# Optimization experiments

Hardware: AMD Instinct MI355X
Metric: run time of the kernel (lower is better)

Reference implementation:

```python
import jax, jax.numpy as jnp
import numpy as np

N = 50000          # nodes
E = 400000         # edges (before self-loops)
F_IN = 64          # node features
H = 256            # hidden_dim
HEADS = 8
HD = 32            # head dim (hidden_dim // 8)
L = 4              # num_layers
G = 64             # num graphs
NGF = 32           # graph features per graph
NC = 2             # classes
EPS = 1e-5


def _bn(x, g, b):
    # BatchNorm1d with batch statistics (training-mode math, no dropout)
    mu = jnp.mean(x, axis=0)
    var = jnp.var(x, axis=0)
    return (x - mu) * jax.lax.rsqrt(var + EPS) * g + b


def _gat(x, src, dst, W, a_src, a_dst, bias):
    # PyG GATConv math (self-loops already included in src/dst)
    h = (x @ W).reshape(N, HEADS, HD)                      # [N,8,32]
    as_n = jnp.sum(h * a_src, axis=-1)                     # [N,8]
    ad_n = jnp.sum(h * a_dst, axis=-1)                     # [N,8]
    e = jax.nn.leaky_relu(as_n[src] + ad_n[dst], 0.2)      # [E',8]
    m = jax.ops.segment_max(e, dst, num_segments=N)        # per-dest softmax
    ex = jnp.exp(e - m[dst])
    den = jax.ops.segment_sum(ex, dst, num_segments=N)
    alpha = ex / den[dst]                                  # [E',8]
    out = jax.ops.segment_sum(alpha[:, :, None] * h[src], dst, num_segments=N)
    return out.reshape(N, HEADS * HD) + bias


def setup_inputs() -> dict:
    key = jax.random.key(0)
    ks = jax.random.split(key, 20)
    s = 0.05
    inp = {
        "x": jax.random.normal(ks[0], (N, F_IN), jnp.float32),
        "edge_index": jax.random.randint(ks[1], (2, E), 0, N, jnp.int32),
        "batch": jnp.sort(jax.random.randint(ks[2], (N,), 0, G, jnp.int32)),
        "graph_features": jax.random.normal(ks[3], (G * NGF,), jnp.float32),
        # node encoder
        "W_enc": jax.random.normal(ks[4], (F_IN, H), jnp.float32) * s,
        "b_enc": jnp.zeros((H,), jnp.float32),
        "g_enc": jnp.ones((H,), jnp.float32),
        "be_enc": jnp.zeros((H,), jnp.float32),
        # GAT layers (stacked over L layers)
        "Wg": jax.random.normal(ks[5], (L, H, H), jnp.float32) * s,
        "att_src": jax.random.normal(ks[6], (L, HEADS, HD), jnp.float32) * s,
        "att_dst": jax.random.normal(ks[7], (L, HEADS, HD), jnp.float32) * s,
        "bg": jnp.zeros((L, H), jnp.float32),
        "bn_g": jnp.ones((L, H), jnp.float32),
        "bn_b": jnp.zeros((L, H), jnp.float32),
        # classifier: (3H + NGF) -> 2H -> H -> NC
        "W1": jax.random.normal(ks[8], (3 * H + NGF, 2 * H), jnp.float32) * s,
        "b1": jnp.zeros((2 * H,), jnp.float32),
        "g1": jnp.ones((2 * H,), jnp.float32),
        "be1": jnp.zeros((2 * H,), jnp.float32),
        "W2": jax.random.normal(ks[9], (2 * H, H), jnp.float32) * s,
        "b2": jnp.zeros((H,), jnp.float32),
        "g2": jnp.ones((H,), jnp.float32),
        "be2": jnp.zeros((H,), jnp.float32),
        "W3": jax.random.normal(ks[10], (H, NC), jnp.float32) * s,
        "b3": jnp.zeros((NC,), jnp.float32),
    }
    return inp


def reference(x, edge_index, batch, graph_features, W_enc, b_enc, g_enc, be_enc,
              Wg, att_src, att_dst, bg, bn_g, bn_b,
              W1, b1, g1, be1, W2, b2, g2, be2, W3, b3):
    gf = graph_features.reshape(G, NGF)
    # add self loops (PyG GATConv default)
    loop = jnp.arange(N, dtype=edge_index.dtype)
    src = jnp.concatenate([edge_index[0], loop])
    dst = jnp.concatenate([edge_index[1], loop])

    h = jax.nn.relu(_bn(x @ W_enc + b_enc, g_enc, be_enc))  # node encoder
    for i in range(L):
        h_in = h
        h = _gat(h, src, dst, Wg[i], att_src[i], att_dst[i], bg[i])
        h = jax.nn.relu(_bn(h, bn_g[i], bn_b[i]))
        if i > 0 and i % 2 == 0:
            h = h + h_in

    # concat pooling: mean / max / sum over graphs
    cnt = jax.ops.segment_sum(jnp.ones((N,), h.dtype), batch, num_segments=G)
    s = jax.ops.segment_sum(h, batch, num_segments=G)
    mean = s / cnt[:, None]
    mx = jax.ops.segment_max(h, batch, num_segments=G)
    pooled = jnp.concatenate([mean, mx, s], axis=1)         # [G, 3H]

    z = jnp.concatenate([pooled, gf], axis=1)               # [G, 3H+NGF]
    z = jax.nn.relu(_bn(z @ W1 + b1, g1, be1))
    z = jax.nn.relu(_bn(z @ W2 + b2, g2, be2))
    return z @ W3 + b3                                      # [G, NC]
```

## Files before the change

kernel.cpp:

```cpp
#include <hip/hip_runtime.h>

#define NN 50000
#define MPAD 50048
#define EE 400000
#define EP 450000
#define FIN 64
#define HH 256
#define GG 64
#define NGFD 32
#define SB 782
#define RB 64

typedef __attribute__((ext_vector_type(8))) _Float16 f16x8;
typedef __attribute__((ext_vector_type(8))) unsigned short u16x8;
typedef __attribute__((ext_vector_type(4))) float f32x4;

__device__ __forceinline__ unsigned short f2h(float f) {
  _Float16 h = (_Float16)f;
  return __builtin_bit_cast(unsigned short, h);
}
__device__ __forceinline__ float h2f(unsigned short s) {
  _Float16 h = __builtin_bit_cast(_Float16, s);
  return (float)h;
}

__global__ void k_init_deg(int* deg) {
  int i = blockIdx.x * 256 + threadIdx.x;
  if (i < NN) deg[i] = 1;
}
__global__ void k_hist(const int* __restrict__ dst, int* __restrict__ deg) {
  int e = blockIdx.x * 256 + threadIdx.x;
  if (e < EE) atomicAdd(&deg[dst[e]], 1);
}
__global__ void k_scan1(const int* __restrict__ deg, int* __restrict__ offs, int* __restrict__ aux) {
  __shared__ int sd[256];
  int b = blockIdx.x, t = threadIdx.x;
  int base = b * 1024 + t * 4;
  int v0 = 0, v1 = 0, v2 = 0, v3 = 0;
  if (base + 0 < NN) v0 = deg[base + 0];
  if (base + 1 < NN) v1 = deg[base + 1];
  if (base + 2 < NN) v2 = deg[base + 2];
  if (base + 3 < NN) v3 = deg[base + 3];
  sd[t] = v0 + v1 + v2 + v3;
  __syncthreads();
  for (int off = 1; off < 256; off <<= 1) {
    int x = (t >= off) ? sd[t - off] : 0;
    __syncthreads();
    sd[t] += x;
    __syncthreads();
  }
  if (t == 255) aux[b] = sd[255];
  int run = (t == 0) ? 0 : sd[t - 1];
  if (base + 0 < NN) offs[base + 0] = run; run += v0;
  if (base + 1 < NN) offs[base + 1] = run; run += v1;
  if (base + 2 < NN) offs[base + 2] = run; run += v2;
  if (base + 3 < NN) offs[base + 3] = run;
}
__global__ void k_scan2(int* aux, int nb) {
  if (threadIdx.x == 0 && blockIdx.x == 0) {
    int s = 0;
    for (int i = 0; i < nb; ++i) { int t = aux[i]; aux[i] = s; s += t; }
    aux[nb] = s;
  }
}
__global__ void k_scan3(int* __restrict__ offs, const int* __restrict__ aux) {
  int b = blockIdx.x, t = threadIdx.x;
  int base = b * 1024 + t * 4;
  int add = aux[b];
  #pragma unroll
  for (int i = 0; i < 4; ++i)
    if (base + i < NN) offs[base + i] += add;
  if (b == 0 && t == 0) offs[NN] = aux[gridDim.x];
}
__global__ void k_scatter(const int* __restrict__ srcA, const int* __restrict__ dstA,
                          int* __restrict__ cur, int* __restrict__ ssrc) {
  int e = blockIdx.x * 256 + threadIdx.x;
  if (e < EE) { int p = atomicAdd(&cur[dstA[e]], 1); ssrc[p] = srcA[e]; }
}
__global__ void k_scatter_self(int* __restrict__ cur, int* __restrict__ ssrc) {
  int i = blockIdx.x * 256 + threadIdx.x;
  if (i < NN) { int p = atomicAdd(&cur[i], 1); ssrc[p] = i; }
}

__global__ void k_bounds(const int* __restrict__ batch, int* __restrict__ start) {
  int g = threadIdx.x;
  if (g > GG) return;
  int lo = 0, hi = NN;
  while (lo < hi) { int mid = (lo + hi) >> 1; if (batch[mid] < g) lo = mid + 1; else hi = mid; }
  start[g] = lo;
}

__global__ void k_prepW(const float* __restrict__ W, unsigned short* __restrict__ WT, int K, int N) {
  __shared__ float tile[32][33];
  int l = blockIdx.z;
  const float* Wp = W + (size_t)l * K * N;
  unsigned short* Tp = WT + (size_t)l * K * N;
  int n0 = blockIdx.x * 32, k0 = blockIdx.y * 32;
  int tx = threadIdx.x & 31, ty = threadIdx.x >> 5;
  #pragma unroll
  for (int rr = 0; rr < 32; rr += 8) {
    int k = k0 + ty + rr, n = n0 + tx;
    if (k < K && n < N) tile[ty + rr][tx] = Wp[(size_t)k * N + n];
  }
  __syncthreads();
  #pragma unroll
  for (int rr = 0; rr < 32; rr += 8) {
    int n = n0 + ty + rr, k = k0 + tx;
    if (n < N && k < K) Tp[(size_t)n * K + k] = f2h(tile[tx][ty + rr]);
  }
}

__global__ void k_cvt_x(const float* __restrict__ x, unsigned short* __restrict__ xb) {
  size_t i = ((size_t)blockIdx.x * 256 + threadIdx.x) * 4;
  if (i >= (size_t)NN * FIN) return;
  float4 v = *reinterpret_cast<const float4*>(x + i);
  ushort4 o;
  o.x = f2h(v.x); o.y = f2h(v.y); o.z = f2h(v.z); o.w = f2h(v.w);
  *reinterpret_cast<ushort4*>(xb + i) = o;
}

__global__ __launch_bounds__(256) void k_mfma(const unsigned short* __restrict__ A,
                                              const unsigned short* __restrict__ BT,
                                              unsigned short* __restrict__ Cb, int K) {
  __shared__ unsigned short Tile[128 * 132];
  unsigned short* As = Tile;
  unsigned short* Bs = Tile + 8192;
  const int t = threadIdx.x;
  const int w = t >> 6, l = t & 63;
  const int row0 = blockIdx.x * 128;
  const int col0 = blockIdx.y * 128;
  const int wm = w & 1, wn = w >> 1;

  f32x4 acc[4][4];
  #pragma unroll
  for (int i = 0; i < 4; ++i)
    #pragma unroll
    for (int j = 0; j < 4; ++j) acc[i][j] = (f32x4){0.f, 0.f, 0.f, 0.f};

  const int lrow = w * 8 + (l >> 3);
  const int ksrc_sh = ((l & 7) ^ (lrow & 7)) << 3;

  for (int k0 = 0; k0 < K; k0 += 64) {
    #pragma unroll
    for (int rd = 0; rd < 4; ++rd) {
      int r = rd * 32 + lrow;
      const unsigned short* ga = A + (size_t)(row0 + r) * K + k0 + ksrc_sh;
      __builtin_amdgcn_global_load_lds(
          (const __attribute__((address_space(1))) void*)ga,
          (__attribute__((address_space(3))) void*)(As + (size_t)(rd * 32 + w * 8) * 64),
          16, 0, 0);
    }
    #pragma unroll
    for (int rd = 0; rd < 4; ++rd) {
      int r = rd * 32 + lrow;
      const unsigned short* gb = BT + (size_t)(col0 + r) * K + k0 + ksrc_sh;
      __builtin_amdgcn_global_load_lds(
          (const __attribute__((address_space(1))) void*)gb,
          (__attribute__((address_space(3))) void*)(Bs + (size_t)(rd * 32 + w * 8) * 64),
          16, 0, 0);
    }
    __syncthreads();

    const char* AsB = (const char*)As;
    const char* BsB = (const char*)Bs;
    #pragma unroll
    for (int ks = 0; ks < 2; ++ks) {
      f16x8 af[4], bfr[4];
      #pragma unroll
      for (int i = 0; i < 4; ++i) {
        int ar = wm * 64 + i * 16 + (l & 15);
        int ab = ar * 128 + ((ks * 64 + (l >> 4) * 16) ^ ((ar & 7) << 4));
        af[i] = *(const f16x8*)(AsB + ab);
        int br = wn * 64 + i * 16 + (l & 15);
        int bb = br * 128 + ((ks * 64 + (l >> 4) * 16) ^ ((br & 7) << 4));
        bfr[i] = *(const f16x8*)(BsB + bb);
      }
      #pragma unroll
      for (int i = 0; i < 4; ++i)
        #pragma unroll
        for (int j = 0; j < 4; ++j)
          acc[i][j] = __builtin_amdgcn_mfma_f32_16x16x32_f16(af[i], bfr[j], acc[i][j], 0, 0, 0);
    }
    __syncthreads();
  }

  #pragma unroll
  for (int i = 0; i < 4; ++i) {
    int lrow2 = wm * 64 + i * 16 + ((l >> 4) * 4);
    #pragma unroll
    for (int j = 0; j < 4; ++j) {
      int lcol = wn * 64 + j * 16 + (l & 15);
      #pragma unroll
      for (int r = 0; r < 4; ++r)
        Tile[(lrow2 + r) * 132 + lcol] = f2h(acc[i][j][r]);
    }
  }
  __syncthreads();
  #pragma unroll
  for (int u = 0; u < 8; ++u) {
    int idx = u * 256 + t;
    int row = idx >> 4;
    int cc  = (idx & 15) * 8;
    int gr = row0 + row;
    if (gr < NN) {
      u16x8 v = *reinterpret_cast<const u16x8*>(&Tile[row * 132 + cc]);
      *reinterpret_cast<u16x8*>(Cb + (size_t)gr * HH + col0 + cc) = v;
    }
  }
}

__global__ void k_attdot(const unsigned short* __restrict__ hp, const float* __restrict__ a_s,
                         const float* __restrict__ a_d, float* __restrict__ asn,
                         float* __restrict__ adn) {
  int lane = threadIdx.x & 63;
  int n = blockIdx.x * 4 + (threadIdx.x >> 6);
  if (n >= NN) return;
  ushort4 v = *reinterpret_cast<const ushort4*>(hp + (size_t)n * HH + lane * 4);
  float4 s4 = *reinterpret_cast<const float4*>(a_s + lane * 4);
  float4 d4 = *reinterpret_cast<const float4*>(a_d + lane * 4);
  float x0 = h2f(v.x), x1 = h2f(v.y), x2 = h2f(v.z), x3 = h2f(v.w);
  float ps = x0 * s4.x + x1 * s4.y + x2 * s4.z + x3 * s4.w;
  float pd = x0 * d4.x + x1 * d4.y + x2 * d4.z + x3 * d4.w;
  ps += __shfl_xor(ps, 1); ps += __shfl_xor(ps, 2); ps += __shfl_xor(ps, 4);
  pd += __shfl_xor(pd, 1); pd += __shfl_xor(pd, 2); pd += __shfl_xor(pd, 4);
  if ((lane & 7) == 0) {
    asn[n * 8 + (lane >> 3)] = ps;
    adn[n * 8 + (lane >> 3)] = pd;
  }
}

__global__ __launch_bounds__(256) void k_gat_agg(const int* __restrict__ offs, const int* __restrict__ ssrc,
                                                 const float* __restrict__ asn, const float* __restrict__ adn,
                                                 const unsigned short* __restrict__ hp,
                                                 unsigned short* __restrict__ outp) {
  int lane = threadIdx.x & 63;
  int n = blockIdx.x * 4 + (threadIdx.x >> 6);
  if (n >= NN) return;
  int hd = lane >> 3;
  float adh = adn[n * 8 + hd];
  int e0 = offs[n], e1 = offs[n + 1];
  float den = 0.f;
  float4 acc = make_float4(0.f, 0.f, 0.f, 0.f);

  auto step = [&](float av, ushort4 hv) {
    float e = fmaxf(av, 0.2f * av);
    float p = __expf(fminf(e, 40.f));
    den += p;
    acc.x += p * h2f(hv.x);
    acc.y += p * h2f(hv.y);
    acc.z += p * h2f(hv.z);
    acc.w += p * h2f(hv.w);
  };

  int k = e0;
  for (; k + 8 <= e1; k += 8) {
    int s[8];
    ushort4 hv[8];
    float a[8];
    #pragma unroll
    for (int u = 0; u < 8; ++u) s[u] = ssrc[k + u];
    #pragma unroll
    for (int u = 0; u < 8; ++u)
      hv[u] = *reinterpret_cast<const ushort4*>(hp + (size_t)s[u] * HH + lane * 4);
    #pragma unroll
    for (int u = 0; u < 8; ++u) a[u] = asn[s[u] * 8 + hd] + adh;
    #pragma unroll
    for (int u = 0; u < 8; ++u) step(a[u], hv[u]);
  }
  for (; k + 4 <= e1; k += 4) {
    int s0 = ssrc[k], s1 = ssrc[k + 1], s2 = ssrc[k + 2], s3 = ssrc[k + 3];
    ushort4 h0 = *reinterpret_cast<const ushort4*>(hp + (size_t)s0 * HH + lane * 4);
    ushort4 h1 = *reinterpret_cast<const ushort4*>(hp + (size_t)s1 * HH + lane * 4);
    ushort4 h2 = *reinterpret_cast<const ushort4*>(hp + (size_t)s2 * HH + lane * 4);
    ushort4 h3 = *reinterpret_cast<const ushort4*>(hp + (size_t)s3 * HH + lane * 4);
    float a0 = asn[s0 * 8 + hd] + adh;
    float a1 = asn[s1 * 8 + hd] + adh;
    float a2 = asn[s2 * 8 + hd] + adh;
    float a3 = asn[s3 * 8 + hd] + adh;
    step(a0, h0); step(a1, h1); step(a2, h2); step(a3, h3);
  }
  for (; k < e1; ++k) {
    int s = ssrc[k];
    ushort4 hv = *reinterpret_cast<const ushort4*>(hp + (size_t)s * HH + lane * 4);
    float av = asn[s * 8 + hd] + adh;
    step(av, hv);
  }
  float rden = 1.f / den;
  ushort4 o;
  o.x = f2h(acc.x * rden); o.y = f2h(acc.y * rden);
  o.z = f2h(acc.z * rden); o.w = f2h(acc.w * rden);
  *reinterpret_cast<ushort4*>(outp + (size_t)n * HH + lane * 4) = o;
}

__global__ void k_cstat_h(const unsigned short* __restrict__ x, float* __restrict__ pst) {
  int c = threadIdx.x, b = blockIdx.x;
  int r0 = b * 64, r1 = min(r0 + 64, NN);
  float s = 0.f, q = 0.f;
  for (int r = r0; r < r1; ++r) {
    float v = h2f(x[(size_t)r * HH + c]);
    s += v; q += v * v;
  }
  pst[b * 512 + c] = s;
  pst[b * 512 + 256 + c] = q;
}
__global__ void k_redstat1(const float* __restrict__ pst, float* __restrict__ pst2) {
  int t = threadIdx.x, p = blockIdx.x;
  int b0 = p * 13, b1 = min(b0 + 13, SB);
  float s0 = 0.f, s1 = 0.f;
  for (int b = b0; b < b1; ++b) {
    s0 += pst[b * 512 + t];
    s1 += pst[b * 512 + 256 + t];
  }
  pst2[p * 512 + t] = s0;
  pst2[p * 512 + 256 + t] = s1;
}
__global__ void k_redstat2(const float* __restrict__ pst2, float* __restrict__ stats) {
  int c = blockIdx.x * 256 + threadIdx.x;
  float s = 0.f;
  #pragma unroll
  for (int b = 0; b < RB; ++b) s += pst2[b * 512 + c];
  stats[c] = s;
}

__global__ void k_bnap_h(const unsigned short* __restrict__ x, const float* __restrict__ stats,
                         const float* __restrict__ g, const float* __restrict__ b,
                         const unsigned short* res, unsigned short* __restrict__ ybf) {
  size_t i = ((size_t)blockIdx.x * 256 + threadIdx.x) * 4;
  if (i >= (size_t)NN * HH) return;
  ushort4 v = *reinterpret_cast<const ushort4*>(x + i);
  int c = (int)(i & 255);
  const float invN = 1.f / (float)NN;
  float vv[4] = {h2f(v.x), h2f(v.y), h2f(v.z), h2f(v.w)};
  float rv[4] = {0.f, 0.f, 0.f, 0.f};
  if (res) {
    ushort4 r4 = *reinterpret_cast<const ushort4*>(res + i);
    rv[0] = h2f(r4.x); rv[1] = h2f(r4.y); rv[2] = h2f(r4.z); rv[3] = h2f(r4.w);
  }
  float o[4];
  #pragma unroll
  for (int j = 0; j < 4; ++j) {
    int cc = c + j;
    float mean = stats[cc] * invN;
    float var = stats[HH + cc] * invN - mean * mean;
    float rs = rsqrtf(var + 1e-5f);
    float val = (vv[j] - mean) * rs * g[cc] + b[cc];
    val = fmaxf(val, 0.f) + rv[j];
    o[j] = val;
  }
  ushort4 bo;
  bo.x = f2h(o[0]); bo.y = f2h(o[1]); bo.z = f2h(o[2]); bo.w = f2h(o[3]);
  *reinterpret_cast<ushort4*>(ybf + i) = bo;
}

__global__ void k_pool(const unsigned short* __restrict__ h, const int* __restrict__ batch,
                       float* __restrict__ gsum, float* __restrict__ gmax) {
  int c = threadIdx.x;
  int r0 = blockIdx.x * 64, r1 = min(r0 + 64, NN);
  if (r0 >= r1) return;
  int curg = batch[r0];
  float s = 0.f, mx = 0.f;
  for (int r = r0; r < r1; ++r) {
    int g = batch[r];
    if (g != curg) {
      atomicAdd(&gsum[curg * HH + c], s);
      atomicMax((int*)&gmax[curg * HH + c], __float_as_int(mx));
      s = 0.f; mx = 0.f; curg = g;
    }
    float v = h2f(h[(size_t)r * HH + c]);
    s += v; mx = fmaxf(mx, v);
  }
  atomicAdd(&gsum[curg * HH + c], s);
  atomicMax((int*)&gmax[curg * HH + c], __float_as_int(mx));
}
__global__ void k_buildz(const float* __restrict__ gsum, const float* __restrict__ gmax,
                         const int* __restrict__ start, const float* __restrict__ gf,
                         float* __restrict__ z) {
  int g = blockIdx.x;
  float invc = 1.f / (float)(start[g + 1] - start[g]);
  for (int c = threadIdx.x; c < 800; c += 256) {
    float v;
    if (c < 256)      v = gsum[g * HH + c] * invc;
    else if (c < 512) v = gmax[g * HH + (c - 256)];
    else if (c < 768) v = gsum[g * HH + (c - 512)];
    else              v = gf[g * NGFD + (c - 768)];
    z[g * 800 + c] = v;
  }
}

__global__ __launch_bounds__(256) void k_linsplit(const float* __restrict__ zin,
                                                  const float* __restrict__ W,
                                                  float* __restrict__ pacc, int K, int OC) {
  __shared__ float zs[64][65];
  int t = threadIdx.x;
  int kc = blockIdx.y, k0 = kc * 64;
  int kmax = min(64, K - k0);
  for (int idx = t; idx < 64 * 64; idx += 256) {
    int r = idx >> 6, k = idx & 63;
    zs[r][k] = (k < kmax) ? zin[(size_t)r * K + k0 + k] : 0.f;
  }
  __syncthreads();
  int jl = t & 15, rq = t >> 4;
  int j = blockIdx.x * 16 + jl;
  float acc[4] = {0.f, 0.f, 0.f, 0.f};
  int k = 0;
  for (; k + 8 <= kmax; k += 8) {
    float wv[8];
    #pragma unroll
    for (int u = 0; u < 8; ++u) wv[u] = W[(size_t)(k0 + k + u) * OC + j];
    #pragma unroll
    for (int u = 0; u < 8; ++u)
      #pragma unroll
      for (int rr = 0; rr < 4; ++rr) acc[rr] += zs[rq * 4 + rr][k + u] * wv[u];
  }
  for (; k < kmax; ++k) {
    float wv = W[(size_t)(k0 + k) * OC + j];
    #pragma unroll
    for (int rr = 0; rr < 4; ++rr) acc[rr] += zs[rq * 4 + rr][k] * wv;
  }
  float* pp = pacc + ((size_t)kc * OC + j) * 64 + rq * 4;
  #pragma unroll
  for (int rr = 0; rr < 4; ++rr) pp[rr] = acc[rr];
}

__global__ __launch_bounds__(64) void k_linred(const float* __restrict__ pacc,
                                               const float* __restrict__ g,
                                               const float* __restrict__ be,
                                               float* __restrict__ zout, int OC, int KC) {
  int j = blockIdx.x, r = threadIdx.x;
  float s = 0.f;
  for (int kc = 0; kc < KC; ++kc) s += pacc[((size_t)kc * OC + j) * 64 + r];
  float S = s, Q = s * s;
  #pragma unroll
  for (int off = 32; off >= 1; off >>= 1) {
    S += __shfl_xor(S, off);
    Q += __shfl_xor(Q, off);
  }
  float mu = S * (1.f / 64.f);
  float var = Q * (1.f / 64.f) - mu * mu;
  float scv = rsqrtf(var + 1e-5f) * g[j];
  float sh = be[j] - mu * scv;
  zout[(size_t)r * OC + j] = fmaxf(s * scv + sh, 0.f);
}

__global__ void k_final(const float* __restrict__ z2, const float* __restrict__ W3,
                        const float* __restrict__ b3, float* __restrict__ out) {
  int t = threadIdx.x;
  if (t >= 128) return;
  int i = t >> 1, j = t & 1;
  float acc = b3[j];
  for (int k = 0; k < 256; ++k) acc += z2[i * 256 + k] * W3[k * 2 + j];
  out[i * 2 + j] = acc;
}

extern "C" void kernel_launch(void* const* d_in, const int* in_sizes, int n_in,
                              void* d_out, int out_size, void* d_ws, size_t ws_size,
                              hipStream_t stream) {
  const float* x      = (const float*)d_in[0];
  const int*   ei     = (const int*)d_in[1];
  const int*   batch  = (const int*)d_in[2];
  const float* gf     = (const float*)d_in[3];
  const float* W_enc  = (const float*)d_in[4];
  const float* g_enc  = (const float*)d_in[6];
  const float* be_enc = (const float*)d_in[7];
  const float* Wg     = (const float*)d_in[8];
  const float* att_s  = (const float*)d_in[9];
  const float* att_d  = (const float*)d_in[10];
  const float* bn_g   = (const float*)d_in[12];
  const float* bn_b   = (const float*)d_in[13];
  const float* W1     = (const float*)d_in[14];
  const float* g1     = (const float*)d_in[16];
  const float* be1    = (const float*)d_in[17];
  const float* W2     = (const float*)d_in[18];
  const float* g2     = (const float*)d_in[20];
  const float* be2    = (const float*)d_in[21];
  const float* W3     = (const float*)d_in[22];
  const float* b3     = (const float*)d_in[23];
  float* out = (float*)d_out;

  char* w = (char*)d_ws;
  auto alloc = [&](size_t bytes) { char* p = w; w += (bytes + 255) & ~(size_t)255; return p; };
  unsigned short* Cc_h = (unsigned short*)alloc((size_t)MPAD * HH * 2);
  unsigned short* A_bf = (unsigned short*)alloc((size_t)MPAD * HH * 2);
  unsigned short* hp   = (unsigned short*)alloc((size_t)MPAD * HH * 2);
  unsigned short* x_bf = (unsigned short*)alloc((size_t)MPAD * FIN * 2);
  float* asn  = (float*)alloc((size_t)NN * 8 * 4);
  float* adn  = (float*)alloc((size_t)NN * 8 * 4);
  int*   deg  = (int*)alloc((size_t)NN * 4);
  int*   offs = (int*)alloc((size_t)(NN + 1) * 4);
  int*   cur  = (int*)alloc((size_t)NN * 4);
  int*   ssrc = (int*)alloc((size_t)EP * 4);
  float* pst  = (float*)alloc((size_t)SB * 512 * 4);
  float* pst2 = (float*)alloc((size_t)RB * 512 * 4);
  float* stats= (float*)alloc(512 * 4);
  int*   aux  = (int*)alloc(64 * 4);
  int*   start= (int*)alloc(65 * 4);
  unsigned short* WencT = (unsigned short*)alloc((size_t)HH * FIN * 2);
  unsigned short* WgT   = (unsigned short*)alloc((size_t)4 * HH * HH * 2);
  float* gsum = (float*)alloc((size_t)GG * HH * 4);
  float* gmax = (float*)alloc((size_t)GG * HH * 4);
  float* zb   = (float*)alloc((size_t)GG * 800 * 4);
  float* z1   = (float*)alloc((size_t)GG * 512 * 4);
  float* z2   = (float*)alloc((size_t)GG * 256 * 4);
  float* pacc = (float*)alloc((size_t)13 * 512 * 64 * 4);

  const int* e_src = ei;
  const int* e_dst = ei + EE;

  k_init_deg<<<196, 256, 0, stream>>>(deg);
  k_hist<<<1563, 256, 0, stream>>>(e_dst, deg);
  k_scan1<<<49, 256, 0, stream>>>(deg, offs, aux);
  k_scan2<<<1, 64, 0, stream>>>(aux, 49);
  k_scan3<<<49, 256, 0, stream>>>(offs, aux);
  hipMemcpyAsync(cur, offs, (size_t)NN * 4, hipMemcpyDeviceToDevice, stream);
  k_scatter<<<1563, 256, 0, stream>>>(e_src, e_dst, cur, ssrc);
  k_scatter_self<<<196, 256, 0, stream>>>(cur, ssrc);
  k_bounds<<<1, 128, 0, stream>>>(batch, start);

  k_prepW<<<dim3(8, 2, 1), 256, 0, stream>>>(W_enc, WencT, FIN, HH);
  k_prepW<<<dim3(8, 8, 4), 256, 0, stream>>>(Wg, WgT, HH, HH);
  k_cvt_x<<<3125, 256, 0, stream>>>(x, x_bf);

  dim3 mg(MPAD / 128, 2);

  k_mfma<<<mg, 256, 0, stream>>>(x_bf, WencT, hp, FIN);
  k_cstat_h<<<SB, 256, 0, stream>>>(hp, pst);
  k_redstat1<<<RB, 256, 0, stream>>>(pst, pst2);
  k_redstat2<<<2, 256, 0, stream>>>(pst2, stats);
  k_bnap_h<<<12500, 256, 0, stream>>>(hp, stats, g_enc, be_enc, nullptr, A_bf);

  for (int l = 0; l < 4; ++l) {
    k_mfma<<<mg, 256, 0, stream>>>(A_bf, WgT + (size_t)l * HH * HH, hp, HH);
    k_attdot<<<12500, 256, 0, stream>>>(hp, att_s + l * HH, att_d + l * HH, asn, adn);
    k_gat_agg<<<12500, 256, 0, stream>>>(offs, ssrc, asn, adn, hp, Cc_h);
    k_cstat_h<<<SB, 256, 0, stream>>>(Cc_h, pst);
    k_redstat1<<<RB, 256, 0, stream>>>(pst, pst2);
    k_redstat2<<<2, 256, 0, stream>>>(pst2, stats);
    k_bnap_h<<<12500, 256, 0, stream>>>(Cc_h, stats, bn_g + l * HH, bn_b + l * HH,
                                        (l == 2) ? A_bf : nullptr, A_bf);
  }

  hipMemsetAsync(gsum, 0, (size_t)GG * HH * 4, stream);
  hipMemsetAsync(gmax, 0, (size_t)GG * HH * 4, stream);
  k_pool<<<SB, 256, 0, stream>>>(A_bf, batch, gsum, gmax);
  k_buildz<<<GG, 256, 0, stream>>>(gsum, gmax, start, gf, zb);
  k_linsplit<<<dim3(32, 13), 256, 0, stream>>>(zb, W1, pacc, 800, 512);
  k_linred<<<512, 64, 0, stream>>>(pacc, g1, be1, z1, 512, 13);
  k_linsplit<<<dim3(16, 8), 256, 0, stream>>>(z1, W2, pacc, 512, 256);
  k_linred<<<256, 64, 0, stream>>>(pacc, g2, be2, z2, 256, 8);
  k_final<<<1, 128, 0, stream>>>(z2, W3, b3, out);
}
```

Before: 612.3 us.

## Fuse attention dot products into GEMM epilogue and drop 8-way gather unroll

Computes the per-head source/destination attention scores inside the MFMA GEMM epilogue from the fp16 output tile held in shared memory, which removes the separate k_attdot kernel and its re-read of the projected features. It also removes the 8-wide unrolled loop in the GAT aggregation so the 4-wide loop handles most edges. The epilogue adds serial 32-element dot products per thread with possible LDS bank conflicts, and the narrower unroll leaves fewer gathers in flight in the aggregation kernel.

```diff
diff --git a/kernel.cpp b/kernel.cpp
--- a/kernel.cpp
+++ b/kernel.cpp
@@ -121,8 +121,13 @@
 
 __global__ __launch_bounds__(256) void k_mfma(const unsigned short* __restrict__ A,
                                               const unsigned short* __restrict__ BT,
-                                              unsigned short* __restrict__ Cb, int K) {
+                                              unsigned short* __restrict__ Cb, int K,
+                                              const float* __restrict__ a_s,
+                                              const float* __restrict__ a_d,
+                                              float* __restrict__ asn,
+                                              float* __restrict__ adn) {
   __shared__ unsigned short Tile[128 * 132];
+  __shared__ float sas[128], sad[128];
   unsigned short* As = Tile;
   unsigned short* Bs = Tile + 8192;
   const int t = threadIdx.x;
@@ -130,6 +135,11 @@
   const int row0 = blockIdx.x * 128;
   const int col0 = blockIdx.y * 128;
   const int wm = w & 1, wn = w >> 1;
+
+  if (a_s && t < 128) {
+    sas[t] = a_s[col0 + t];
+    sad[t] = a_d[col0 + t];
+  }
 
   f32x4 acc[4][4];
   #pragma unroll
@@ -196,6 +206,7 @@
     }
   }
   __syncthreads();
+
   #pragma unroll
   for (int u = 0; u < 8; ++u) {
     int idx = u * 256 + t;
@@ -207,25 +218,29 @@
       *reinterpret_cast<u16x8*>(Cb + (size_t)gr * HH + col0 + cc) = v;
     }
   }
-}
-
-__global__ void k_attdot(const unsigned short* __restrict__ hp, const float* __restrict__ a_s,
-                         const float* __restrict__ a_d, float* __restrict__ asn,
-                         float* __restrict__ adn) {
-  int lane = threadIdx.x & 63;
-  int n = blockIdx.x * 4 + (threadIdx.x >> 6);
-  if (n >= NN) return;
-  ushort4 v = *reinterpret_cast<const ushort4*>(hp + (size_t)n * HH + lane * 4);
-  float4 s4 = *reinterpret_cast<const float4*>(a_s + lane * 4);
-  float4 d4 = *reinterpret_cast<const float4*>(a_d + lane * 4);
-  float x0 = h2f(v.x), x1 = h2f(v.y), x2 = h2f(v.z), x3 = h2f(v.w);
-  float ps = x0 * s4.x + x1 * s4.y + x2 * s4.z + x3 * s4.w;
-  float pd = x0 * d4.x + x1 * d4.y + x2 * d4.z + x3 * d4.w;
-  ps += __shfl_xor(ps, 1); ps += __shfl_xor(ps, 2); ps += __shfl_xor(ps, 4);
-  pd += __shfl_xor(pd, 1); pd += __shfl_xor(pd, 2); pd += __shfl_xor(pd, 4);
-  if ((lane & 7) == 0) {
-    asn[n * 8 + (lane >> 3)] = ps;
-    adn[n * 8 + (lane >> 3)] = pd;
+
+  if (a_s) {
+    int hbase = col0 >> 5;
+    #pragma unroll
+    for (int pp = 0; pp < 2; ++pp) {
+      int p = pp * 256 + t;
+      int row = p >> 2, hh = p & 3;
+      int gr = row0 + row;
+      if (gr < NN) {
+        const unsigned short* rp = &Tile[row * 132 + hh * 32];
+        const float* asp = &sas[hh * 32];
+        const float* adp = &sad[hh * 32];
+        float ps = 0.f, pd = 0.f;
+        #pragma unroll
+        for (int c = 0; c < 32; ++c) {
+          float hv = h2f(rp[c]);
+          ps += hv * asp[c];
+          pd += hv * adp[c];
+        }
+        asn[gr * 8 + hbase + hh] = ps;
+        adn[gr * 8 + hbase + hh] = pd;
+      }
+    }
   }
 }
 
@@ -253,20 +268,6 @@
   };
 
   int k = e0;
-  for (; k + 8 <= e1; k += 8) {
-    int s[8];
-    ushort4 hv[8];
-    float a[8];
-    #pragma unroll
-    for (int u = 0; u < 8; ++u) s[u] = ssrc[k + u];
-    #pragma unroll
-    for (int u = 0; u < 8; ++u)
-      hv[u] = *reinterpret_cast<const ushort4*>(hp + (size_t)s[u] * HH + lane * 4);
-    #pragma unroll
-    for (int u = 0; u < 8; ++u) a[u] = asn[s[u] * 8 + hd] + adh;
-    #pragma unroll
-    for (int u = 0; u < 8; ++u) step(a[u], hv[u]);
-  }
   for (; k + 4 <= e1; k += 4) {
     int s0 = ssrc[k], s1 = ssrc[k + 1], s2 = ssrc[k + 2], s3 = ssrc[k + 3];
     ushort4 h0 = *reinterpret_cast<const ushort4*>(hp + (size_t)s0 * HH + lane * 4);
@@ -522,15 +523,15 @@
 
   dim3 mg(MPAD / 128, 2);
 
-  k_mfma<<<mg, 256, 0, stream>>>(x_bf, WencT, hp, FIN);
+  k_mfma<<<mg, 256, 0, stream>>>(x_bf, WencT, hp, FIN, nullptr, nullptr, nullptr, nullptr);
   k_cstat_h<<<SB, 256, 0, stream>>>(hp, pst);
   k_redstat1<<<RB, 256, 0, stream>>>(pst, pst2);
   k_redstat2<<<2, 256, 0, stream>>>(pst2, stats);
   k_bnap_h<<<12500, 256, 0, stream>>>(hp, stats, g_enc, be_enc, nullptr, A_bf);
 
   for (int l = 0; l < 4; ++l) {
-    k_mfma<<<mg, 256, 0, stream>>>(A_bf, WgT + (size_t)l * HH * HH, hp, HH);
-    k_attdot<<<12500, 256, 0, stream>>>(hp, att_s + l * HH, att_d + l * HH, asn, adn);
+    k_mfma<<<mg, 256, 0, stream>>>(A_bf, WgT + (size_t)l * HH * HH, hp, HH,
+                                   att_s + l * HH, att_d + l * HH, asn, adn);
     k_gat_agg<<<12500, 256, 0, stream>>>(offs, ssrc, asn, adn, hp, Cc_h);
     k_cstat_h<<<SB, 256, 0, stream>>>(Cc_h, pst);
     k_redstat1<<<RB, 256, 0, stream>>>(pst, pst2);
```

After: 585.6 us, median of 2. 4.4% less time.
